# Kernel optimization log

Measured on AMD Instinct MI355X. Metric: run time of the kernel, lower is better.

Reference implementation:

```python
import jax, jax.numpy as jnp
import numpy as np

H = 8
DK = 16  # 128 // 8
DM = 128


def setup_inputs() -> dict:
    key = jax.random.key(0)
    ks = jax.random.split(key, 12)
    B, S = 4, 2048
    inp = {
        "query": jax.random.normal(ks[0], (B, S, DM), dtype=jnp.float32),
        "key": jax.random.normal(ks[1], (B, S, DM), dtype=jnp.float32),
        "value": jax.random.normal(ks[2], (B, S, DM), dtype=jnp.float32),
        "pos_embed": jax.random.normal(ks[3], (B, S, DM), dtype=jnp.float32),
        # three projection linears (shared: L0 for pos_query & query, L1 for pos_key & key, L2 for value)
        "W0": jax.random.normal(ks[4], (DM, DM), dtype=jnp.float32) / np.sqrt(DM),
        "b0": jnp.zeros((DM,), dtype=jnp.float32),
        "W1": jax.random.normal(ks[5], (DM, DM), dtype=jnp.float32) / np.sqrt(DM),
        "b1": jnp.zeros((DM,), dtype=jnp.float32),
        "W2": jax.random.normal(ks[6], (DM, DM), dtype=jnp.float32) / np.sqrt(DM),
        "b2": jnp.zeros((DM,), dtype=jnp.float32),
        "Wo": jax.random.normal(ks[7], (DM, DM), dtype=jnp.float32) / np.sqrt(DM),
        "bo": jnp.zeros((DM,), dtype=jnp.float32),
    }
    return inp


def _proj(x, W, b):
    # Linear then split heads: [B,S,128] -> [B,H,S,DK]
    B = x.shape[0]
    y = x @ W.T + b
    return y.reshape(B, -1, H, DK).transpose(0, 2, 1, 3)


def reference(query, key, value, pos_embed, W0, b0, W1, b1, W2, b2, Wo, bo):
    B = query.shape[0]
    pos1 = pos_embed[..., 0:DM]
    pos_q = _proj(pos1, W0, b0)  # shares L0 with query proj (as in source zip bug)
    pos_k = _proj(pos1, W1, b1)
    pos_attn = jnp.einsum("bhqd,bhkd->bhqk", pos_q, pos_k)  # [B,H,S,S]

    q = _proj(query, W0, b0)
    k = _proj(key, W1, b1)
    v = _proj(value, W2, b2)

    scale = 1.0 / jnp.sqrt(jnp.asarray(DK, dtype=q.dtype))
    scores = jnp.einsum("bhqd,bhkd->bhqk", q, k) * scale + pos_attn
    attn = jax.nn.softmax(scores, axis=-1)  # dropout = identity (eval)
    x = jnp.einsum("bhqk,bhkd->bhqd", attn, v)  # [B,H,S,DK]
    x = x.transpose(0, 2, 1, 3).reshape(B, -1, H * DK)
    return x @ Wo.T + bo
```

## Files before the change

### kernel.cpp

```cpp
#include <hip/hip_runtime.h>
#include <math.h>

#define LOG2E 1.44269504088896340736f

typedef __attribute__((ext_vector_type(8))) short bfrag;
typedef __attribute__((ext_vector_type(4))) float f4;
typedef unsigned __attribute__((ext_vector_type(2))) u2;

__device__ __forceinline__ unsigned pk_trunc(float a, float b) {
#if __has_builtin(__builtin_amdgcn_perm)
    return __builtin_amdgcn_perm(__float_as_uint(b), __float_as_uint(a), 0x07060302u);
#else
    return (__float_as_uint(a) >> 16) | (__float_as_uint(b) & 0xFFFF0000u);
#endif
}
__device__ __forceinline__ unsigned pk_rne(float a, float b) {
    unsigned ua = __float_as_uint(a); ua += 0x7FFFu + ((ua >> 16) & 1u);
    unsigned ub = __float_as_uint(b); ub += 0x7FFFu + ((ub >> 16) & 1u);
    return (ua >> 16) | (ub & 0xFFFF0000u);
}
__device__ __forceinline__ float trunchi(float x) {
    return __uint_as_float(__float_as_uint(x) & 0xFFFF0000u);
}
__device__ __forceinline__ float fexp2(float x) {
#if __has_builtin(__builtin_amdgcn_exp2f)
    return __builtin_amdgcn_exp2f(x);
#else
    return exp2f(x);
#endif
}
__device__ __forceinline__ void plswap16(float& a, float& b) {
#if __has_builtin(__builtin_amdgcn_permlane16_swap)
    u2 t = __builtin_amdgcn_permlane16_swap(__float_as_uint(a), __float_as_uint(b),
                                            false, false);
    a = __uint_as_float(t.x); b = __uint_as_float(t.y);
#else
    bool odd = (threadIdx.x >> 4) & 1;
    float bs = __shfl_xor(b, 16, 64);
    float as = __shfl_xor(a, 16, 64);
    float na = odd ? bs : a;
    float nb = odd ? b : as;
    a = na; b = nb;
#endif
}
__device__ __forceinline__ void stage16(void* lds_base, const void* g) {
#if __has_builtin(__builtin_amdgcn_global_load_lds)
    __builtin_amdgcn_global_load_lds(
        (const __attribute__((address_space(1))) unsigned int*)g,
        (__attribute__((address_space(3))) unsigned int*)lds_base, 16, 0, 0);
#else
    int lane = threadIdx.x & 63;
    *(float4*)((char*)lds_base + lane * 16) = *(const float4*)g;
#endif
}
__device__ __forceinline__ f4 mfma_bf16(bfrag a, bfrag b, f4 c) {
    return __builtin_amdgcn_mfma_f32_16x16x32_bf16(a, b, c, 0, 0, 0);
}
__device__ __forceinline__ void conv8(const float* __restrict__ g, bfrag& hi, bfrag& lo) {
    f4 a = *(const f4*)g;
    f4 b = *(const f4*)(g + 4);
    union { unsigned u[4]; bfrag v; } H, L;
    H.u[0] = pk_trunc(a.x, a.y); H.u[1] = pk_trunc(a.z, a.w);
    H.u[2] = pk_trunc(b.x, b.y); H.u[3] = pk_trunc(b.z, b.w);
    L.u[0] = pk_trunc(a.x - trunchi(a.x), a.y - trunchi(a.y));
    L.u[1] = pk_trunc(a.z - trunchi(a.z), a.w - trunchi(a.w));
    L.u[2] = pk_trunc(b.x - trunchi(b.x), b.y - trunchi(b.y));
    L.u[3] = pk_trunc(b.z - trunchi(b.z), b.w - trunchi(b.w));
    hi = H.v; lo = L.v;
}
__device__ __forceinline__ void store_q(f4 ea, f4 eb, char* base, int lodelta, int lane) {
    float eah[4], eal[4], ebh[4], ebl[4];
#pragma unroll
    for (int r = 0; r < 4; ++r) {
        eah[r] = trunchi(ea[r]); eal[r] = ea[r] - eah[r];
        ebh[r] = trunchi(eb[r]); ebl[r] = eb[r] - ebh[r];
    }
#pragma unroll
    for (int r = 0; r < 4; ++r) { plswap16(eah[r], ebh[r]); plswap16(eal[r], ebl[r]); }
    union { unsigned u[4]; bfrag v; } H, L;
    H.u[0] = pk_trunc(eah[0], eah[1]); H.u[1] = pk_trunc(eah[2], eah[3]);
    H.u[2] = pk_trunc(ebh[0], ebh[1]); H.u[3] = pk_trunc(ebh[2], ebh[3]);
    L.u[0] = pk_trunc(eal[0], eal[1]); L.u[1] = pk_trunc(eal[2], eal[3]);
    L.u[2] = pk_trunc(ebl[0], ebl[1]); L.u[3] = pk_trunc(ebl[2], ebl[3]);
    *(bfrag*)(base + lane * 16) = H.v;
    *(bfrag*)(base + lodelta + lane * 16) = L.v;
}
__device__ __forceinline__ void store_rne(f4 ea, f4 eb, char* base, int lane) {
    float a[4], b[4];
#pragma unroll
    for (int r = 0; r < 4; ++r) { a[r] = ea[r]; b[r] = eb[r]; }
#pragma unroll
    for (int r = 0; r < 4; ++r) plswap16(a[r], b[r]);
    union { unsigned u[4]; bfrag v; } P;
    P.u[0] = pk_rne(a[0], a[1]); P.u[1] = pk_rne(a[2], a[3]);
    P.u[2] = pk_rne(b[0], b[1]); P.u[3] = pk_rne(b[2], b[3]);
    *(bfrag*)(base + lane * 16) = P.v;
}

#define WS_QB 0u
#define WS_KV 8388608u
#define WS_X  14680064u
#define WS_WI 18874368u

__global__ __launch_bounds__(256) void w_prep(
    const float* __restrict__ W0, const float* __restrict__ W1,
    const float* __restrict__ W2, const float* __restrict__ Wo,
    char* __restrict__ wimg)
{
    int wid = blockIdx.x * 4 + (threadIdx.x >> 6);
    int lane = threadIdx.x & 63;
    int img = wid >> 5, rem = wid & 31, tile = rem >> 2, kg = rem & 3;
    const float* W = (img <= 1) ? W0 : (img == 2) ? W1 : (img == 3) ? W2 : Wo;
    float s = (img == 0) ? 0.25f * LOG2E : (img == 1) ? LOG2E : 1.0f;
    int n = lane & 15, qd = lane >> 4;
    const float* g = W + (size_t)(tile * 16 + n) * 128 + kg * 32 + qd * 8;
    f4 a = *(const f4*)g, b = *(const f4*)(g + 4);
    a.x *= s; a.y *= s; a.z *= s; a.w *= s;
    b.x *= s; b.y *= s; b.z *= s; b.w *= s;
    union { unsigned u[4]; bfrag v; } H, L;
    H.u[0] = pk_trunc(a.x, a.y); H.u[1] = pk_trunc(a.z, a.w);
    H.u[2] = pk_trunc(b.x, b.y); H.u[3] = pk_trunc(b.z, b.w);
    L.u[0] = pk_trunc(a.x - trunchi(a.x), a.y - trunchi(a.y));
    L.u[1] = pk_trunc(a.z - trunchi(a.z), a.w - trunchi(a.w));
    L.u[2] = pk_trunc(b.x - trunchi(b.x), b.y - trunchi(b.y));
    L.u[3] = pk_trunc(b.z - trunchi(b.z), b.w - trunchi(b.w));
    char* dst = wimg + img * 65536 + tile * 8192 + kg * 2048;
    *(bfrag*)(dst + lane * 16) = H.v;
    *(bfrag*)(dst + 1024 + lane * 16) = L.v;
}

__global__ __launch_bounds__(256) void k_proj(
    const float* __restrict__ query, const float* __restrict__ key,
    const float* __restrict__ value, const float* __restrict__ pos,
    const float* __restrict__ b0, const float* __restrict__ b1,
    const float* __restrict__ b2,
    const char* __restrict__ wimg, char* __restrict__ qb, char* __restrict__ kv)
{
    __shared__ __align__(16) char xlds[65536];
    const int tid = threadIdx.x;
    const int bid = blockIdx.x;
    const int b = bid >> 6, s32 = bid & 63;
    const size_t rowbase = (size_t)(b * 2048 + s32 * 32);

#pragma unroll
    for (int i = 0; i < 8; ++i) {
        int cid = tid + i * 256;
        int arr = cid >> 9, rem = cid & 511;
        int c32 = rem >> 4, u = rem & 15;
        const float* sp = (arr == 0) ? query : (arr == 1) ? key
                        : (arr == 2) ? value : pos;
        bfrag hi, lo;
        conv8(sp + (rowbase + c32) * 128 + u * 8, hi, lo);
        int base = arr * 16384 + (c32 >> 4) * 8192 + (u >> 2) * 2048
                 + ((u & 3) * 16 + (c32 & 15)) * 16;
        *(bfrag*)(xlds + base) = hi;
        *(bfrag*)(xlds + base + 1024) = lo;
    }
    __syncthreads();

    const int w = tid >> 6, lane = tid & 63;
    const int n = lane & 15, qd = lane >> 4;
#pragma unroll
    for (int hh = 0; hh < 2; ++hh) {
        const int h = w * 2 + hh;
        const int bh = b * 8 + h;
        {
            bfrag wqh[4], wql[4], wph[4], wpl[4];
#pragma unroll
            for (int kg = 0; kg < 4; ++kg) {
                const char* wb = wimg + 0 * 65536 + h * 8192 + kg * 2048;
                wqh[kg] = *(const bfrag*)(wb + lane * 16);
                wql[kg] = *(const bfrag*)(wb + 1024 + lane * 16);
                const char* pb = wimg + 1 * 65536 + h * 8192 + kg * 2048;
                wph[kg] = *(const bfrag*)(pb + lane * 16);
                wpl[kg] = *(const bfrag*)(pb + 1024 + lane * 16);
            }
            float bq[4], bp[4];
#pragma unroll
            for (int r = 0; r < 4; ++r) {
                float bv = b0[h * 16 + qd * 4 + r];
                bq[r] = 0.25f * LOG2E * bv; bp[r] = LOG2E * bv;
            }
#pragma unroll
            for (int pp = 0; pp < 2; ++pp) {
                f4 cq = {bq[0], bq[1], bq[2], bq[3]};
                f4 cp = {bp[0], bp[1], bp[2], bp[3]};
#pragma unroll
                for (int kg = 0; kg < 4; ++kg) {
                    const char* xq = xlds + 0 * 16384 + pp * 8192 + kg * 2048 + lane * 16;
                    const char* xp = xlds + 3 * 16384 + pp * 8192 + kg * 2048 + lane * 16;
                    bfrag xh = *(const bfrag*)xq, xl = *(const bfrag*)(xq + 1024);
                    bfrag ph = *(const bfrag*)xp, pl = *(const bfrag*)(xp + 1024);
                    cq = mfma_bf16(wqh[kg], xh, cq);
                    cq = mfma_bf16(wqh[kg], xl, cq);
                    cq = mfma_bf16(wql[kg], xh, cq);
                    cp = mfma_bf16(wph[kg], ph, cp);
                    cp = mfma_bf16(wph[kg], pl, cp);
                    cp = mfma_bf16(wpl[kg], ph, cp);
                }
                int pg = s32 * 2 + pp;
                store_q(cq, cp, qb + (size_t)bh * 262144 + (size_t)pg * 2048, 1024, lane);
            }
        }
        {
            bfrag w1h[4], w1l[4];
#pragma unroll
            for (int kg = 0; kg < 4; ++kg) {
                const char* wb = wimg + 2 * 65536 + h * 8192 + kg * 2048;
                w1h[kg] = *(const bfrag*)(wb + lane * 16);
                w1l[kg] = *(const bfrag*)(wb + 1024 + lane * 16);
            }
            float bk[4];
#pragma unroll
            for (int r = 0; r < 4; ++r) bk[r] = b1[h * 16 + qd * 4 + r];
#pragma unroll
            for (int pp = 0; pp < 2; ++pp) {
                f4 ck = {bk[0], bk[1], bk[2], bk[3]};
                f4 cpk = {bk[0], bk[1], bk[2], bk[3]};
#pragma unroll
                for (int kg = 0; kg < 4; ++kg) {
                    const char* xk = xlds + 1 * 16384 + pp * 8192 + kg * 2048 + lane * 16;
                    const char* xp = xlds + 3 * 16384 + pp * 8192 + kg * 2048 + lane * 16;
                    bfrag xh = *(const bfrag*)xk, xl = *(const bfrag*)(xk + 1024);
                    bfrag ph = *(const bfrag*)xp, pl = *(const bfrag*)(xp + 1024);
                    ck = mfma_bf16(w1h[kg], xh, ck);
                    ck = mfma_bf16(w1h[kg], xl, ck);
                    ck = mfma_bf16(w1l[kg], xh, ck);
                    cpk = mfma_bf16(w1h[kg], ph, cpk);
                    cpk = mfma_bf16(w1h[kg], pl, cpk);
                    cpk = mfma_bf16(w1l[kg], ph, cpk);
                }
                int pg = s32 * 2 + pp;
                store_rne(ck, cpk,
                          kv + (size_t)bh * 196608 + (size_t)(pg >> 3) * 12288
                          + (pg & 7) * 1024, lane);
            }
        }
        {
            bfrag w2h[4], w2l[4];
#pragma unroll
            for (int kg = 0; kg < 4; ++kg) {
                const char* wb = wimg + 3 * 65536 + h * 8192 + kg * 2048;
                w2h[kg] = *(const bfrag*)(wb + lane * 16);
                w2l[kg] = *(const bfrag*)(wb + 1024 + lane * 16);
            }
            float bv = b2[h * 16 + n];
            f4 ca = {bv, bv, bv, bv};
            f4 cb = {bv, bv, bv, bv};
#pragma unroll
            for (int pp = 0; pp < 2; ++pp) {
#pragma unroll
                for (int kg = 0; kg < 4; ++kg) {
                    const char* xv = xlds + 2 * 16384 + pp * 8192 + kg * 2048 + lane * 16;
                    bfrag ah = *(const bfrag*)xv, al = *(const bfrag*)(xv + 1024);
                    if (pp == 0) {
                        ca = mfma_bf16(ah, w2h[kg], ca);
                        ca = mfma_bf16(al, w2h[kg], ca);
                        ca = mfma_bf16(ah, w2l[kg], ca);
                    } else {
                        cb = mfma_bf16(ah, w2h[kg], cb);
                        cb = mfma_bf16(al, w2h[kg], cb);
                        cb = mfma_bf16(ah, w2l[kg], cb);
                    }
                }
            }
            store_rne(ca, cb,
                      kv + (size_t)bh * 196608 + (size_t)(s32 >> 2) * 12288
                      + 8192 + (s32 & 3) * 1024, lane);
        }
    }
}

__global__ __launch_bounds__(256) void k_attn(
    const char* __restrict__ qb, const char* __restrict__ kvg,
    float* __restrict__ xout)
{
    __shared__ __align__(16) char kbuf[2][12288];
    const int tid = threadIdx.x;
    const int w = tid >> 6, lane = tid & 63;
    const int c = lane & 15, qd = lane >> 4;
    const int bh = blockIdx.y;
    const int q0 = blockIdx.x * 128 + w * 32;

    const char* qpb = qb + (size_t)bh * 262144 + (size_t)(q0 >> 4) * 2048;
    bfrag qh0 = *(const bfrag*)(qpb + lane * 16);
    bfrag ql0 = *(const bfrag*)(qpb + 1024 + lane * 16);
    bfrag qh1 = *(const bfrag*)(qpb + 2048 + lane * 16);
    bfrag ql1 = *(const bfrag*)(qpb + 3072 + lane * 16);

    const char* kvb = kvg + (size_t)bh * 196608;

    union { unsigned u[4]; bfrag v; } onesu;
    onesu.u[0] = 0x3F803F80u; onesu.u[1] = 0x3F803F80u;
    onesu.u[2] = 0x3F803F80u; onesu.u[3] = 0x3F803F80u;
    const bfrag ones = onesu.v;

    f4 o0 = {0.f, 0.f, 0.f, 0.f}, o1 = {0.f, 0.f, 0.f, 0.f};
    f4 l0 = {0.f, 0.f, 0.f, 0.f}, l1 = {0.f, 0.f, 0.f, 0.f};

    auto stage = [&](char* db, const char* gsrc) {
        stage16(db + w * 2048, gsrc + w * 2048 + lane * 16);
        stage16(db + w * 2048 + 1024, gsrc + w * 2048 + 1024 + lane * 16);
        stage16(db + 8192 + w * 1024, gsrc + 8192 + w * 1024 + lane * 16);
    };

    stage(kbuf[0], kvb);
    const char* gnext = kvb + 12288;
    int cur = 0;
    for (int ch = 0; ch < 16; ++ch) {
        asm volatile("s_waitcnt vmcnt(0)" ::: "memory");
        __syncthreads();
        if (ch < 15) { stage(kbuf[cur ^ 1], gnext); gnext += 12288; }
        const char* kb = kbuf[cur];
#pragma unroll
        for (int sub = 0; sub < 4; ++sub) {
            bfrag ka = *(const bfrag*)(kb + (2 * sub) * 1024 + lane * 16);
            bfrag kc2 = *(const bfrag*)(kb + (2 * sub + 1) * 1024 + lane * 16);
            bfrag vf = *(const bfrag*)(kb + 8192 + sub * 1024 + lane * 16);
            {
                f4 sa = {0.f, 0.f, 0.f, 0.f}, sb = {0.f, 0.f, 0.f, 0.f};
                sa = mfma_bf16(ka, qh0, sa);  sa = mfma_bf16(ka, ql0, sa);
                sb = mfma_bf16(kc2, qh0, sb); sb = mfma_bf16(kc2, ql0, sb);
                float ea[4], eb[4];
#pragma unroll
                for (int r = 0; r < 4; ++r) { ea[r] = fexp2(sa[r]); eb[r] = fexp2(sb[r]); }
#pragma unroll
                for (int r = 0; r < 4; ++r) plswap16(ea[r], eb[r]);
                union { unsigned u[4]; bfrag v; } pf;
                pf.u[0] = pk_trunc(ea[0], ea[1]); pf.u[1] = pk_trunc(ea[2], ea[3]);
                pf.u[2] = pk_trunc(eb[0], eb[1]); pf.u[3] = pk_trunc(eb[2], eb[3]);
                o0 = mfma_bf16(pf.v, vf, o0);
                l0 = mfma_bf16(pf.v, ones, l0);
            }
            {
                f4 sa = {0.f, 0.f, 0.f, 0.f}, sb = {0.f, 0.f, 0.f, 0.f};
                sa = mfma_bf16(ka, qh1, sa);  sa = mfma_bf16(ka, ql1, sa);
                sb = mfma_bf16(kc2, qh1, sb); sb = mfma_bf16(kc2, ql1, sb);
                float ea[4], eb[4];
#pragma unroll
                for (int r = 0; r < 4; ++r) { ea[r] = fexp2(sa[r]); eb[r] = fexp2(sb[r]); }
#pragma unroll
                for (int r = 0; r < 4; ++r) plswap16(ea[r], eb[r]);
                union { unsigned u[4]; bfrag v; } pf;
                pf.u[0] = pk_trunc(ea[0], ea[1]); pf.u[1] = pk_trunc(ea[2], ea[3]);
                pf.u[2] = pk_trunc(eb[0], eb[1]); pf.u[3] = pk_trunc(eb[2], eb[3]);
                o1 = mfma_bf16(pf.v, vf, o1);
                l1 = mfma_bf16(pf.v, ones, l1);
            }
        }
        cur ^= 1;
    }

    const int bbk = bh >> 3, h = bh & 7;
#pragma unroll
    for (int r = 0; r < 4; ++r) {
        int row = qd * 4 + r;
        xout[((size_t)(bbk * 2048 + q0 + row)) * 128 + h * 16 + c] = o0[r] / l0[r];
        xout[((size_t)(bbk * 2048 + q0 + 16 + row)) * 128 + h * 16 + c] = o1[r] / l1[r];
    }
}

__global__ __launch_bounds__(128) void k_out(
    const float* __restrict__ x, const char* __restrict__ wimg,
    const float* __restrict__ bo, float* __restrict__ out)
{
    const int tid = threadIdx.x;
    const int w = tid >> 6, lane = tid & 63;
    const int n = lane & 15, qd = lane >> 4;
    const int row0 = blockIdx.x * 16;

    bfrag xh[4], xl[4];
#pragma unroll
    for (int kg = 0; kg < 4; ++kg)
        conv8(x + (size_t)(row0 + n) * 128 + kg * 32 + qd * 8, xh[kg], xl[kg]);

#pragma unroll
    for (int tt = 0; tt < 4; ++tt) {
        int t = w * 4 + tt;
        float bv = bo[t * 16 + n];
        f4 cacc = {bv, bv, bv, bv};
#pragma unroll
        for (int kg = 0; kg < 4; ++kg) {
            const char* wb = wimg + 4 * 65536 + t * 8192 + kg * 2048;
            bfrag wh = *(const bfrag*)(wb + lane * 16);
            bfrag wl = *(const bfrag*)(wb + 1024 + lane * 16);
            cacc = mfma_bf16(xh[kg], wh, cacc);
            cacc = mfma_bf16(xl[kg], wh, cacc);
            cacc = mfma_bf16(xh[kg], wl, cacc);
        }
#pragma unroll
        for (int r = 0; r < 4; ++r)
            out[(size_t)(row0 + qd * 4 + r) * 128 + t * 16 + n] = cacc[r];
    }
}

extern "C" void kernel_launch(void* const* d_in, const int* in_sizes, int n_in,
                              void* d_out, int out_size, void* d_ws, size_t ws_size,
                              hipStream_t stream)
{
    const float* query = (const float*)d_in[0];
    const float* key   = (const float*)d_in[1];
    const float* value = (const float*)d_in[2];
    const float* pos   = (const float*)d_in[3];
    const float* W0 = (const float*)d_in[4];
    const float* b0 = (const float*)d_in[5];
    const float* W1 = (const float*)d_in[6];
    const float* b1 = (const float*)d_in[7];
    const float* W2 = (const float*)d_in[8];
    const float* b2 = (const float*)d_in[9];
    const float* Wo = (const float*)d_in[10];
    const float* bo = (const float*)d_in[11];

    char* ws = (char*)d_ws;
    char* qbuf = ws + WS_QB;
    char* kv   = ws + WS_KV;
    float* x   = (float*)(ws + WS_X);
    char* wimg = ws + WS_WI;
    float* out = (float*)d_out;

    w_prep<<<dim3(40), 256, 0, stream>>>(W0, W1, W2, Wo, wimg);
    k_proj<<<dim3(256), 256, 0, stream>>>(query, key, value, pos, b0, b1, b2,
                                          wimg, qbuf, kv);
    k_attn<<<dim3(16, 32), 256, 0, stream>>>(qbuf, kv, x);
    k_out<<<dim3(512), 128, 0, stream>>>(x, wimg, bo, out);
}
```

Measured before the change: 132.2 us.

## Transpose attention MFMA operands to drop lane swaps and emit bf16 x panels

The attention P·V product is recomputed transposed (V as the A operand, probabilities as B), which removes the permlane16 swaps around the exp/pack step. Q/K/V stores drop their swaps to match the new fragment layout. The attention output is now written as RNE-rounded bf16 MFMA-ready panels instead of fp32 rows, so k_out loads fragments directly and needs two MFMAs per step instead of three. The Wo image layout and the attention block size (128 threads, more blocks) are adjusted to fit. In exchange, the output projection input loses its low-order correction term, which costs some accuracy.

```diff
diff --git a/kernel.cpp b/kernel.cpp
--- a/kernel.cpp
+++ b/kernel.cpp
@@ -27,20 +27,6 @@
     return __builtin_amdgcn_exp2f(x);
 #else
     return exp2f(x);
-#endif
-}
-__device__ __forceinline__ void plswap16(float& a, float& b) {
-#if __has_builtin(__builtin_amdgcn_permlane16_swap)
-    u2 t = __builtin_amdgcn_permlane16_swap(__float_as_uint(a), __float_as_uint(b),
-                                            false, false);
-    a = __uint_as_float(t.x); b = __uint_as_float(t.y);
-#else
-    bool odd = (threadIdx.x >> 4) & 1;
-    float bs = __shfl_xor(b, 16, 64);
-    float as = __shfl_xor(a, 16, 64);
-    float na = odd ? bs : a;
-    float nb = odd ? b : as;
-    a = na; b = nb;
 #endif
 }
 __device__ __forceinline__ void stage16(void* lds_base, const void* g) {
@@ -68,32 +54,21 @@
     L.u[3] = pk_trunc(b.z - trunchi(b.z), b.w - trunchi(b.w));
     hi = H.v; lo = L.v;
 }
-__device__ __forceinline__ void store_q(f4 ea, f4 eb, char* base, int lodelta, int lane) {
-    float eah[4], eal[4], ebh[4], ebl[4];
-#pragma unroll
-    for (int r = 0; r < 4; ++r) {
-        eah[r] = trunchi(ea[r]); eal[r] = ea[r] - eah[r];
-        ebh[r] = trunchi(eb[r]); ebl[r] = eb[r] - ebh[r];
-    }
-#pragma unroll
-    for (int r = 0; r < 4; ++r) { plswap16(eah[r], ebh[r]); plswap16(eal[r], ebl[r]); }
+__device__ __forceinline__ void store_q2(f4 ea, f4 eb, char* base, int lodelta, int lane) {
     union { unsigned u[4]; bfrag v; } H, L;
-    H.u[0] = pk_trunc(eah[0], eah[1]); H.u[1] = pk_trunc(eah[2], eah[3]);
-    H.u[2] = pk_trunc(ebh[0], ebh[1]); H.u[3] = pk_trunc(ebh[2], ebh[3]);
-    L.u[0] = pk_trunc(eal[0], eal[1]); L.u[1] = pk_trunc(eal[2], eal[3]);
-    L.u[2] = pk_trunc(ebl[0], ebl[1]); L.u[3] = pk_trunc(ebl[2], ebl[3]);
+    H.u[0] = pk_trunc(ea[0], ea[1]); H.u[1] = pk_trunc(ea[2], ea[3]);
+    H.u[2] = pk_trunc(eb[0], eb[1]); H.u[3] = pk_trunc(eb[2], eb[3]);
+    L.u[0] = pk_trunc(ea[0] - trunchi(ea[0]), ea[1] - trunchi(ea[1]));
+    L.u[1] = pk_trunc(ea[2] - trunchi(ea[2]), ea[3] - trunchi(ea[3]));
+    L.u[2] = pk_trunc(eb[0] - trunchi(eb[0]), eb[1] - trunchi(eb[1]));
+    L.u[3] = pk_trunc(eb[2] - trunchi(eb[2]), eb[3] - trunchi(eb[3]));
     *(bfrag*)(base + lane * 16) = H.v;
     *(bfrag*)(base + lodelta + lane * 16) = L.v;
 }
-__device__ __forceinline__ void store_rne(f4 ea, f4 eb, char* base, int lane) {
-    float a[4], b[4];
-#pragma unroll
-    for (int r = 0; r < 4; ++r) { a[r] = ea[r]; b[r] = eb[r]; }
-#pragma unroll
-    for (int r = 0; r < 4; ++r) plswap16(a[r], b[r]);
+__device__ __forceinline__ void store_rne2(f4 ea, f4 eb, char* base, int lane) {
     union { unsigned u[4]; bfrag v; } P;
-    P.u[0] = pk_rne(a[0], a[1]); P.u[1] = pk_rne(a[2], a[3]);
-    P.u[2] = pk_rne(b[0], b[1]); P.u[3] = pk_rne(b[2], b[3]);
+    P.u[0] = pk_rne(ea[0], ea[1]); P.u[1] = pk_rne(ea[2], ea[3]);
+    P.u[2] = pk_rne(eb[0], eb[1]); P.u[3] = pk_rne(eb[2], eb[3]);
     *(bfrag*)(base + lane * 16) = P.v;
 }
 
@@ -113,8 +88,10 @@
     const float* W = (img <= 1) ? W0 : (img == 2) ? W1 : (img == 3) ? W2 : Wo;
     float s = (img == 0) ? 0.25f * LOG2E : (img == 1) ? LOG2E : 1.0f;
     int n = lane & 15, qd = lane >> 4;
-    const float* g = W + (size_t)(tile * 16 + n) * 128 + kg * 32 + qd * 8;
-    f4 a = *(const f4*)g, b = *(const f4*)(g + 4);
+    const float* rowp = W + (size_t)(tile * 16 + n) * 128 + kg * 32;
+    f4 a, b;
+    if (img == 4) { a = *(const f4*)(rowp + qd * 4); b = *(const f4*)(rowp + 16 + qd * 4); }
+    else          { a = *(const f4*)(rowp + qd * 8); b = *(const f4*)(rowp + qd * 8 + 4); }
     a.x *= s; a.y *= s; a.z *= s; a.w *= s;
     b.x *= s; b.y *= s; b.z *= s; b.w *= s;
     union { unsigned u[4]; bfrag v; } H, L;
@@ -199,7 +176,7 @@
                     cp = mfma_bf16(wpl[kg], ph, cp);
                 }
                 int pg = s32 * 2 + pp;
-                store_q(cq, cp, qb + (size_t)bh * 262144 + (size_t)pg * 2048, 1024, lane);
+                store_q2(cq, cp, qb + (size_t)bh * 262144 + (size_t)pg * 2048, 1024, lane);
             }
         }
         {
@@ -231,9 +208,9 @@
                     cpk = mfma_bf16(w1l[kg], ph, cpk);
                 }
                 int pg = s32 * 2 + pp;
-                store_rne(ck, cpk,
-                          kv + (size_t)bh * 196608 + (size_t)(pg >> 3) * 12288
-                          + (pg & 7) * 1024, lane);
+                store_rne2(ck, cpk,
+                           kv + (size_t)bh * 196608 + (size_t)(pg >> 3) * 12288
+                           + (pg & 7) * 1024, lane);
             }
         }
         {
@@ -264,23 +241,22 @@
                     }
                 }
             }
-            store_rne(ca, cb,
-                      kv + (size_t)bh * 196608 + (size_t)(s32 >> 2) * 12288
-                      + 8192 + (s32 & 3) * 1024, lane);
+            store_rne2(ca, cb,
+                       kv + (size_t)bh * 196608 + (size_t)(s32 >> 2) * 12288
+                       + 8192 + (s32 & 3) * 1024, lane);
         }
     }
 }
 
-__global__ __launch_bounds__(256) void k_attn(
+__global__ __launch_bounds__(128) void k_attn(
     const char* __restrict__ qb, const char* __restrict__ kvg,
-    float* __restrict__ xout)
+    char* __restrict__ xb)
 {
     __shared__ __align__(16) char kbuf[2][12288];
     const int tid = threadIdx.x;
     const int w = tid >> 6, lane = tid & 63;
-    const int c = lane & 15, qd = lane >> 4;
     const int bh = blockIdx.y;
-    const int q0 = blockIdx.x * 128 + w * 32;
+    const int q0 = blockIdx.x * 64 + w * 32;
 
     const char* qpb = qb + (size_t)bh * 262144 + (size_t)(q0 >> 4) * 2048;
     bfrag qh0 = *(const bfrag*)(qpb + lane * 16);
@@ -299,9 +275,9 @@
     f4 l0 = {0.f, 0.f, 0.f, 0.f}, l1 = {0.f, 0.f, 0.f, 0.f};
 
     auto stage = [&](char* db, const char* gsrc) {
-        stage16(db + w * 2048, gsrc + w * 2048 + lane * 16);
-        stage16(db + w * 2048 + 1024, gsrc + w * 2048 + 1024 + lane * 16);
-        stage16(db + 8192 + w * 1024, gsrc + 8192 + w * 1024 + lane * 16);
+#pragma unroll
+        for (int i = 0; i < 6; ++i)
+            stage16(db + (w * 6 + i) * 1024, gsrc + (w * 6 + i) * 1024 + lane * 16);
     };
 
     stage(kbuf[0], kvb);
@@ -321,62 +297,58 @@
                 f4 sa = {0.f, 0.f, 0.f, 0.f}, sb = {0.f, 0.f, 0.f, 0.f};
                 sa = mfma_bf16(ka, qh0, sa);  sa = mfma_bf16(ka, ql0, sa);
                 sb = mfma_bf16(kc2, qh0, sb); sb = mfma_bf16(kc2, ql0, sb);
-                float ea[4], eb[4];
-#pragma unroll
-                for (int r = 0; r < 4; ++r) { ea[r] = fexp2(sa[r]); eb[r] = fexp2(sb[r]); }
-#pragma unroll
-                for (int r = 0; r < 4; ++r) plswap16(ea[r], eb[r]);
                 union { unsigned u[4]; bfrag v; } pf;
-                pf.u[0] = pk_trunc(ea[0], ea[1]); pf.u[1] = pk_trunc(ea[2], ea[3]);
-                pf.u[2] = pk_trunc(eb[0], eb[1]); pf.u[3] = pk_trunc(eb[2], eb[3]);
-                o0 = mfma_bf16(pf.v, vf, o0);
-                l0 = mfma_bf16(pf.v, ones, l0);
+                pf.u[0] = pk_trunc(fexp2(sa[0]), fexp2(sa[1]));
+                pf.u[1] = pk_trunc(fexp2(sa[2]), fexp2(sa[3]));
+                pf.u[2] = pk_trunc(fexp2(sb[0]), fexp2(sb[1]));
+                pf.u[3] = pk_trunc(fexp2(sb[2]), fexp2(sb[3]));
+                o0 = mfma_bf16(vf, pf.v, o0);
+                l0 = mfma_bf16(ones, pf.v, l0);
             }
             {
                 f4 sa = {0.f, 0.f, 0.f, 0.f}, sb = {0.f, 0.f, 0.f, 0.f};
                 sa = mfma_bf16(ka, qh1, sa);  sa = mfma_bf16(ka, ql1, sa);
                 sb = mfma_bf16(kc2, qh1, sb); sb = mfma_bf16(kc2, ql1, sb);
-                float ea[4], eb[4];
-#pragma unroll
-                for (int r = 0; r < 4; ++r) { ea[r] = fexp2(sa[r]); eb[r] = fexp2(sb[r]); }
-#pragma unroll
-                for (int r = 0; r < 4; ++r) plswap16(ea[r], eb[r]);
                 union { unsigned u[4]; bfrag v; } pf;
-                pf.u[0] = pk_trunc(ea[0], ea[1]); pf.u[1] = pk_trunc(ea[2], ea[3]);
-                pf.u[2] = pk_trunc(eb[0], eb[1]); pf.u[3] = pk_trunc(eb[2], eb[3]);
-                o1 = mfma_bf16(pf.v, vf, o1);
-                l1 = mfma_bf16(pf.v, ones, l1);
+                pf.u[0] = pk_trunc(fexp2(sa[0]), fexp2(sa[1]));
+                pf.u[1] = pk_trunc(fexp2(sa[2]), fexp2(sa[3]));
+                pf.u[2] = pk_trunc(fexp2(sb[0]), fexp2(sb[1]));
+                pf.u[3] = pk_trunc(fexp2(sb[2]), fexp2(sb[3]));
+                o1 = mfma_bf16(vf, pf.v, o1);
+                l1 = mfma_bf16(ones, pf.v, l1);
             }
         }
         cur ^= 1;
     }
 
     const int bbk = bh >> 3, h = bh & 7;
-#pragma unroll
-    for (int r = 0; r < 4; ++r) {
-        int row = qd * 4 + r;
-        xout[((size_t)(bbk * 2048 + q0 + row)) * 128 + h * 16 + c] = o0[r] / l0[r];
-        xout[((size_t)(bbk * 2048 + q0 + 16 + row)) * 128 + h * 16 + c] = o1[r] / l1[r];
-    }
+    const int gp0 = bbk * 128 + (q0 >> 4);
+    char* xw = xb + (size_t)gp0 * 4096 + (h >> 1) * 1024 + lane * 16 + (h & 1) * 8;
+    float inv0 = 1.0f / l0[0];
+    float inv1 = 1.0f / l1[0];
+    u2 s0 = {pk_rne(o0[0] * inv0, o0[1] * inv0), pk_rne(o0[2] * inv0, o0[3] * inv0)};
+    u2 s1 = {pk_rne(o1[0] * inv1, o1[1] * inv1), pk_rne(o1[2] * inv1, o1[3] * inv1)};
+    *(u2*)xw = s0;
+    *(u2*)(xw + 4096) = s1;
 }
 
 __global__ __launch_bounds__(128) void k_out(
-    const float* __restrict__ x, const char* __restrict__ wimg,
+    const char* __restrict__ xb, const char* __restrict__ wimg,
     const float* __restrict__ bo, float* __restrict__ out)
 {
     const int tid = threadIdx.x;
     const int w = tid >> 6, lane = tid & 63;
     const int n = lane & 15, qd = lane >> 4;
-    const int row0 = blockIdx.x * 16;
-
-    bfrag xh[4], xl[4];
+    const int panel = blockIdx.x * 2 + w;
+    const int row0 = panel * 16;
+
+    bfrag xf[4];
 #pragma unroll
     for (int kg = 0; kg < 4; ++kg)
-        conv8(x + (size_t)(row0 + n) * 128 + kg * 32 + qd * 8, xh[kg], xl[kg]);
-
-#pragma unroll
-    for (int tt = 0; tt < 4; ++tt) {
-        int t = w * 4 + tt;
+        xf[kg] = *(const bfrag*)(xb + (size_t)panel * 4096 + kg * 1024 + lane * 16);
+
+#pragma unroll
+    for (int t = 0; t < 8; ++t) {
         float bv = bo[t * 16 + n];
         f4 cacc = {bv, bv, bv, bv};
 #pragma unroll
@@ -384,9 +356,8 @@
             const char* wb = wimg + 4 * 65536 + t * 8192 + kg * 2048;
             bfrag wh = *(const bfrag*)(wb + lane * 16);
             bfrag wl = *(const bfrag*)(wb + 1024 + lane * 16);
-            cacc = mfma_bf16(xh[kg], wh, cacc);
-            cacc = mfma_bf16(xl[kg], wh, cacc);
-            cacc = mfma_bf16(xh[kg], wl, cacc);
+            cacc = mfma_bf16(xf[kg], wh, cacc);
+            cacc = mfma_bf16(xf[kg], wl, cacc);
         }
 #pragma unroll
         for (int r = 0; r < 4; ++r)
@@ -414,13 +385,13 @@
     char* ws = (char*)d_ws;
     char* qbuf = ws + WS_QB;
     char* kv   = ws + WS_KV;
-    float* x   = (float*)(ws + WS_X);
+    char* xbuf = ws + WS_X;
     char* wimg = ws + WS_WI;
     float* out = (float*)d_out;
 
     w_prep<<<dim3(40), 256, 0, stream>>>(W0, W1, W2, Wo, wimg);
     k_proj<<<dim3(256), 256, 0, stream>>>(query, key, value, pos, b0, b1, b2,
                                           wimg, qbuf, kv);
-    k_attn<<<dim3(16, 32), 256, 0, stream>>>(qbuf, kv, x);
-    k_out<<<dim3(512), 128, 0, stream>>>(x, wimg, bo, out);
-}
+    k_attn<<<dim3(32, 32), 128, 0, stream>>>(qbuf, kv, xbuf);
+    k_out<<<dim3(256), 128, 0, stream>>>(xbuf, wimg, bo, out);
+}
```

New measurement: 128.6 us. -2.7%, faster.
